# Kernel tuning notes

Measured on AMD Instinct MI355X. Metric: run time of the kernel, lower is better.

The kernel has to match this reference:

```python
import jax, jax.numpy as jnp
import numpy as np

B, C, H, W = 8, 512, 32, 32
NH = 8


def setup_inputs() -> dict:
    key = jax.random.key(0)
    ks = jax.random.split(key, 10)
    s = 1.0 / np.sqrt(C)
    return {
        "query": jax.random.normal(ks[0], (B, C, H, W), jnp.float32),
        "key": jax.random.normal(ks[1], (B, C, H, W), jnp.float32),
        "Wq": jax.random.normal(ks[2], (C, C), jnp.float32) * s,
        "bq": jnp.zeros((C,), jnp.float32),
        "Wk": jax.random.normal(ks[3], (C, C), jnp.float32) * s,
        "bk": jnp.zeros((C,), jnp.float32),
        "Wv": jax.random.normal(ks[4], (C, C), jnp.float32) * s,
        "bv": jnp.zeros((C,), jnp.float32),
        "Wo": jax.random.normal(ks[5], (C, C), jnp.float32) * s,
        "bo": jnp.zeros((C,), jnp.float32),
        "num_heads": NH,
    }


def reference(query, key, Wq, bq, Wk, bk, Wv, bv, Wo, bo, num_heads):
    b, c, h, w = query.shape
    hd = c // num_heads
    scale = hd ** (-0.5)
    # [B,C,H,W] -> [B, L, C] with L = H*W
    qf = jnp.transpose(query, (0, 2, 3, 1)).reshape(b, -1, c)
    kf = jnp.transpose(key, (0, 2, 3, 1)).reshape(b, -1, c)
    L = qf.shape[1]
    # Linear projections (torch Linear: x @ W.T + b); value = key
    q = qf @ Wq.T + bq
    k = kf @ Wk.T + bk
    v = kf @ Wv.T + bv
    # split heads: [B, L, NH, hd] -> [B, NH, L, hd]
    q = q.reshape(b, L, num_heads, hd).transpose(0, 2, 1, 3) * scale
    k = k.reshape(b, L, num_heads, hd).transpose(0, 2, 1, 3)
    v = v.reshape(b, L, num_heads, hd).transpose(0, 2, 1, 3)
    scores = jnp.einsum('bhqd,bhkd->bhqk', q, k)
    attn = jax.nn.softmax(scores, axis=-1)  # dropout p=0.0 -> identity
    o = jnp.einsum('bhqk,bhkd->bhqd', attn, v)
    o = o.transpose(0, 2, 1, 3).reshape(b, L, c)
    o = o @ Wo.T + bo
    o = o + qf + kf  # residual with flattened query and key
    return jnp.transpose(o.reshape(b, h, w, c), (0, 3, 1, 2))
```

## Files before the change

kernel.cpp:

```cpp
#include <hip/hip_runtime.h>
#include <stdint.h>

#define B_  8
#define C_  512
#define L_  1024
#define NH_ 8
#define HD_ 64

typedef __attribute__((ext_vector_type(8))) short short8;
typedef __attribute__((ext_vector_type(4))) short short4v;
typedef __attribute__((ext_vector_type(4))) float f32x4;
typedef __attribute__((ext_vector_type(2))) unsigned uint2v;

#define MFMA(a,b,c) __builtin_amdgcn_mfma_f32_16x16x32_bf16((a),(b),(c),0,0,0)
#define GLD16(g,l) __builtin_amdgcn_global_load_lds( \
    (const __attribute__((address_space(1))) void*)(g), \
    (__attribute__((address_space(3))) void*)(l), 16, 0, 0)

__device__ __forceinline__ unsigned short f2bf(float f) {
  union { float f; unsigned u; } x; x.f = f;
  unsigned r = x.u + 0x7FFFu + ((x.u >> 16) & 1u);
  return (unsigned short)(r >> 16);
}

__device__ __forceinline__ unsigned cvtpk_bf16(float lo, float hi) {
  unsigned r;
  asm("v_cvt_pk_bf16_f32 %0, %1, %2" : "=v"(r) : "v"(lo), "v"(hi));
  return r;
}

__global__ __launch_bounds__(256) void k_transpose(
    const float* __restrict__ q, const float* __restrict__ k,
    unsigned short* __restrict__ qf, unsigned short* __restrict__ kf) {
  __shared__ float t[32][33];
  const int z = blockIdx.z;
  const int b = z >> 1;
  const float* src = (z & 1) ? k : q;
  unsigned short* dst = (z & 1) ? kf : qf;
  const int tx = threadIdx.x & 31;
  const int ty = threadIdx.x >> 5;
  const int l0 = blockIdx.x * 32;
  const int c0 = blockIdx.y * 32;
#pragma unroll
  for (int i = 0; i < 4; ++i)
    t[ty + 8*i][tx] = src[((size_t)b * C_ + c0 + ty + 8*i) * L_ + l0 + tx];
  __syncthreads();
#pragma unroll
  for (int i = 0; i < 4; ++i)
    dst[((size_t)b * L_ + l0 + ty + 8*i) * C_ + c0 + tx] = f2bf(t[tx][ty + 8*i]);
}

__global__ __launch_bounds__(256) void k_convw(
    const float* __restrict__ w0, const float* __restrict__ w1,
    const float* __restrict__ w2, const float* __restrict__ w3,
    unsigned short* __restrict__ dst) {
  const int z = blockIdx.y;
  const float* s = (z == 0) ? w0 : (z == 1) ? w1 : (z == 2) ? w2 : w3;
  unsigned short* d = dst + (size_t)z * (C_ * C_);
  const int i = (blockIdx.x * 256 + threadIdx.x) * 4;
  float4 v = *(const float4*)&s[i];
  short4v p;
  p[0] = (short)f2bf(v.x); p[1] = (short)f2bf(v.y);
  p[2] = (short)f2bf(v.z); p[3] = (short)f2bf(v.w);
  *(short4v*)&d[i] = p;
}

template<int MREP>
__device__ __forceinline__ void gemm_core(
    const unsigned short* __restrict__ A, const unsigned short* __restrict__ W,
    const float* __restrict__ bias, void* __restrict__ outp,
    const float* __restrict__ resQ, const float* __restrict__ resK,
    int mode, float scale, unsigned short* lA, unsigned short* lB,
    int tm, int tn) {
  const int lane = threadIdx.x & 63;
  const int wid  = threadIdx.x >> 6;
  const int wm = wid >> 1, wn = wid & 1;
  const int r16 = lane & 15;
  const int g4  = lane >> 4;

  f32x4 acc[MREP][4];
#pragma unroll
  for (int i = 0; i < MREP; ++i)
#pragma unroll
    for (int j = 0; j < 4; ++j) acc[i][j] = (f32x4){0.f, 0.f, 0.f, 0.f};

  for (int kt = 0; kt < C_; kt += 64) {
#pragma unroll
    for (int i = 0; i < MREP; ++i) {
      int chunk = wid * MREP + i;
      int row = chunk * 8 + (lane >> 3);
      int col = (lane & 7) * 8;
      GLD16(A + (size_t)(tm + row) * C_ + kt + col, &lA[chunk * 512]);
    }
#pragma unroll
    for (int i = 0; i < 4; ++i) {
      int chunk = wid * 4 + i;
      int row = chunk * 8 + (lane >> 3);
      int col = (lane & 7) * 8;
      GLD16(W + (size_t)(tn + row) * C_ + kt + col, &lB[chunk * 512]);
    }
    __syncthreads();
#pragma unroll
    for (int ks = 0; ks < 2; ++ks) {
      const int co = ks * 32 + g4 * 8;
      short8 af[MREP], bw[4];
#pragma unroll
      for (int i = 0; i < MREP; ++i)
        af[i] = *(const short8*)&lA[(wm*(MREP*16) + i*16 + r16) * 64 + co];
#pragma unroll
      for (int j = 0; j < 4; ++j) bw[j] = *(const short8*)&lB[(wn*64 + j*16 + r16) * 64 + co];
#pragma unroll
      for (int i = 0; i < MREP; ++i)
#pragma unroll
        for (int j = 0; j < 4; ++j) acc[i][j] = MFMA(af[i], bw[j], acc[i][j]);
    }
    __syncthreads();
  }

  if (mode <= 1) {
    unsigned short* out = (unsigned short*)outp;
#pragma unroll
    for (int i = 0; i < MREP; ++i)
#pragma unroll
      for (int j = 0; j < 4; ++j) {
        int c = tn + wn*64 + j*16 + r16;
        float bia = bias[c];
        int h = c >> 6, d = c & 63;
#pragma unroll
        for (int r = 0; r < 4; ++r) {
          int gm = tm + wm*(MREP*16) + i*16 + g4*4 + r;
          int b = gm >> 10, l = gm & 1023;
          out[(((size_t)b * NH_ + h) * L_ + l) * HD_ + d] = f2bf((acc[i][j][r] + bia) * scale);
        }
      }
  } else if (mode == 2) {
    unsigned short* out = (unsigned short*)outp;
#pragma unroll
    for (int i = 0; i < MREP; ++i)
#pragma unroll
      for (int j = 0; j < 4; ++j) {
        int c = tn + wn*64 + j*16 + r16;
        float bia = bias[c];
        int h = c >> 6, d = c & 63;
        int gm0 = tm + wm*(MREP*16) + i*16 + g4*4;
        int b = gm0 >> 10, l0 = gm0 & 1023;
        short4v pk;
#pragma unroll
        for (int r = 0; r < 4; ++r) pk[r] = (short)f2bf(acc[i][j][r] + bia);
        *(short4v*)&out[(((size_t)b * NH_ + h) * HD_ + d) * L_ + l0] = pk;
      }
  } else {
    float* out = (float*)outp;
#pragma unroll
    for (int i = 0; i < MREP; ++i)
#pragma unroll
      for (int j = 0; j < 4; ++j) {
        int c = tn + wn*64 + j*16 + r16;
        float bia = bias[c];
        int gm0 = tm + wm*(MREP*16) + i*16 + g4*4;
        int b = gm0 >> 10, l0 = gm0 & 1023;
        size_t idx = ((size_t)b * C_ + c) * L_ + l0;
        float4 q4 = *(const float4*)&resQ[idx];
        float4 k4 = *(const float4*)&resK[idx];
        float4 o4;
        o4.x = acc[i][j][0] + bia + q4.x + k4.x;
        o4.y = acc[i][j][1] + bia + q4.y + k4.y;
        o4.z = acc[i][j][2] + bia + q4.z + k4.z;
        o4.w = acc[i][j][3] + bia + q4.w + k4.w;
        *(float4*)&out[idx] = o4;
      }
  }
}

__global__ __launch_bounds__(256) void k_proj(
    const unsigned short* __restrict__ qf, const unsigned short* __restrict__ kf,
    const unsigned short* __restrict__ Wqb, const unsigned short* __restrict__ Wkb,
    const unsigned short* __restrict__ Wvb,
    const float* __restrict__ bq, const float* __restrict__ bk, const float* __restrict__ bv,
    unsigned short* __restrict__ Qw, unsigned short* __restrict__ Kw,
    unsigned short* __restrict__ VTw) {
  __shared__ unsigned short lA[128 * 64];
  __shared__ unsigned short lB[128 * 64];
  const int bid = blockIdx.x;
  const int xcd = bid & 7;
  const int i_  = bid >> 3;
  const int ml  = i_ / 12;
  const int rem = i_ - ml * 12;
  const int z   = rem >> 2;
  const int n   = rem & 3;
  const int m   = xcd * 8 + ml;
  const unsigned short* A = (z == 0) ? qf : kf;
  const unsigned short* W = (z == 0) ? Wqb : (z == 1) ? Wkb : Wvb;
  const float* bias = (z == 0) ? bq : (z == 1) ? bk : bv;
  void* out = (z == 0) ? (void*)Qw : (z == 1) ? (void*)Kw : (void*)VTw;
  float scale = (z == 0) ? 0.125f * 1.44269504088896f : 1.0f;
  gemm_core<4>(A, W, bias, out, nullptr, nullptr, z, scale, lA, lB, m * 128, n * 128);
}

__global__ __launch_bounds__(256) void k_outproj(
    const unsigned short* __restrict__ O, const unsigned short* __restrict__ Wob,
    const float* __restrict__ bo, float* __restrict__ out,
    const float* __restrict__ query, const float* __restrict__ key) {
  __shared__ unsigned short lA[64 * 64];
  __shared__ unsigned short lB[128 * 64];
  const int bid = blockIdx.x;
  const int xcd = bid & 7;
  const int i_  = bid >> 3;
  const int m   = xcd * 16 + (i_ >> 2);
  const int n   = i_ & 3;
  gemm_core<2>(O, Wob, bo, out, query, key, 3, 1.0f, lA, lB, m * 64, n * 128);
}

__global__ __launch_bounds__(256, 2) void k_attn(
    const unsigned short* __restrict__ Q, const unsigned short* __restrict__ K,
    const unsigned short* __restrict__ VT, unsigned short* __restrict__ O) {
  __shared__ unsigned short Kt[2][64 * 64];
  __shared__ unsigned short Vt[2][64 * 64];
  __shared__ __align__(16) unsigned short Pl[4][32 * 36];
  const int lane = threadIdx.x & 63;
  const int wid  = threadIdx.x >> 6;
  const int bid  = blockIdx.x;
  const int xcd  = bid & 7;
  const int i_   = bid >> 3;
  const int bh   = xcd * 8 + (i_ >> 3);
  const int qb   = i_ & 7;
  const int qrow0 = qb * 128 + wid * 32;
  const int r16 = lane & 15;
  const int g4  = lane >> 4;
  const size_t base = (size_t)bh * L_ * HD_;
  const unsigned short* Kg = K + base;
  const unsigned short* Vg = VT + base;

  const int s0 = wid * 128 + lane;
  const int row0 = s0 >> 3,        ch0 = (s0 & 7) ^ (row0 & 7);
  const int row1 = (s0 + 64) >> 3, ch1 = ((s0 + 64) & 7) ^ (row1 & 7);

#define STAGE_KV(nxt, kt0) { \
    GLD16(Kg + (size_t)((kt0) + row0) * HD_ + ch0 * 8, &Kt[nxt][(wid*128)*8]); \
    GLD16(Kg + (size_t)((kt0) + row1) * HD_ + ch1 * 8, &Kt[nxt][(wid*128+64)*8]); \
    GLD16(Vg + (size_t)row0 * L_ + (kt0) + ch0 * 8, &Vt[nxt][(wid*128)*8]); \
    GLD16(Vg + (size_t)row1 * L_ + (kt0) + ch1 * 8, &Vt[nxt][(wid*128+64)*8]); \
  }

  short8 qv[2][2];
#pragma unroll
  for (int i = 0; i < 2; ++i)
#pragma unroll
    for (int ks = 0; ks < 2; ++ks)
      qv[i][ks] = *(const short8*)(Q + base + (size_t)(qrow0 + i*16 + r16) * HD_ + ks*32 + g4*8);

  short8 vones;
#pragma unroll
  for (int e = 0; e < 8; ++e) vones[e] = (short)0x3F80;

  f32x4 lacc[2];
  f32x4 oacc[2][4];
#pragma unroll
  for (int i = 0; i < 2; ++i) {
    lacc[i] = (f32x4){0.f, 0.f, 0.f, 0.f};
#pragma unroll
    for (int j = 0; j < 4; ++j) oacc[i][j] = (f32x4){0.f, 0.f, 0.f, 0.f};
  }

  unsigned short* myP = &Pl[wid][0];

  STAGE_KV(0, 0);
  __syncthreads();

  int cur = 0;
  for (int t = 0; t < 16; ++t) {
    if (t < 15) STAGE_KV(cur ^ 1, (t + 1) * 64);

    const unsigned short* lK = &Kt[cur][0];
    const unsigned short* lV = &Vt[cur][0];

    f32x4 sc[2][4];
#pragma unroll
    for (int i = 0; i < 2; ++i)
#pragma unroll
      for (int cf = 0; cf < 4; ++cf) sc[i][cf] = (f32x4){0.f, 0.f, 0.f, 0.f};

    const int swz = r16 & 7;
    __builtin_amdgcn_s_setprio(1);
#pragma unroll
    for (int cf = 0; cf < 4; ++cf) {
      const int rowb = (cf*16 + r16) * 64;
      short8 kb0 = *(const short8*)&lK[rowb + ((g4) ^ swz) * 8];
      short8 kb1 = *(const short8*)&lK[rowb + ((4 + g4) ^ swz) * 8];
      sc[0][cf] = MFMA(kb0, qv[0][0], sc[0][cf]);
      sc[0][cf] = MFMA(kb1, qv[0][1], sc[0][cf]);
      sc[1][cf] = MFMA(kb0, qv[1][0], sc[1][cf]);
      sc[1][cf] = MFMA(kb1, qv[1][1], sc[1][cf]);
    }
    __builtin_amdgcn_s_setprio(0);

#pragma unroll
    for (int half = 0; half < 2; ++half) {
#pragma unroll
      for (int i = 0; i < 2; ++i)
#pragma unroll
        for (int cfl = 0; cfl < 2; ++cfl) {
          const int cf = half * 2 + cfl;
          float p0 = exp2f(sc[i][cf][0]);
          float p1 = exp2f(sc[i][cf][1]);
          float p2 = exp2f(sc[i][cf][2]);
          float p3 = exp2f(sc[i][cf][3]);
          uint2v pk;
          pk[0] = cvtpk_bf16(p0, p1);
          pk[1] = cvtpk_bf16(p2, p3);
          *(uint2v*)&myP[(i*16 + r16) * 36 + cfl * 16 + g4 * 4] = pk;
        }
      short8 pa0 = *(const short8*)&myP[r16 * 36 + g4 * 8];
      short8 pa1 = *(const short8*)&myP[(16 + r16) * 36 + g4 * 8];
      __builtin_amdgcn_s_setprio(1);
      lacc[0] = MFMA(pa0, vones, lacc[0]);
      lacc[1] = MFMA(pa1, vones, lacc[1]);
#pragma unroll
      for (int j = 0; j < 4; ++j) {
        short8 vb = *(const short8*)&lV[(j*16 + r16) * 64 + ((half*4 + g4) ^ swz) * 8];
        oacc[0][j] = MFMA(pa0, vb, oacc[0][j]);
        oacc[1][j] = MFMA(pa1, vb, oacc[1][j]);
      }
      __builtin_amdgcn_s_setprio(0);
    }

    __syncthreads();
    cur ^= 1;
  }

  const int b = bh >> 3, h = bh & 7;
#pragma unroll
  for (int i = 0; i < 2; ++i) {
    float linv[4];
#pragma unroll
    for (int r = 0; r < 4; ++r) linv[r] = 1.0f / lacc[i][r];
#pragma unroll
    for (int j = 0; j < 4; ++j)
#pragma unroll
      for (int r = 0; r < 4; ++r) {
        int row = qrow0 + i*16 + g4*4 + r;
        int col = h*64 + j*16 + r16;
        O[((size_t)b * L_ + row) * C_ + col] = f2bf(oacc[i][j][r] * linv[r]);
      }
  }
#undef STAGE_KV
}

extern "C" void kernel_launch(void* const* d_in, const int* in_sizes, int n_in,
                              void* d_out, int out_size, void* d_ws, size_t ws_size,
                              hipStream_t stream) {
  (void)in_sizes; (void)n_in; (void)out_size; (void)ws_size;
  const float* query = (const float*)d_in[0];
  const float* key   = (const float*)d_in[1];
  const float* Wq = (const float*)d_in[2];
  const float* bq = (const float*)d_in[3];
  const float* Wk = (const float*)d_in[4];
  const float* bk = (const float*)d_in[5];
  const float* Wv = (const float*)d_in[6];
  const float* bv = (const float*)d_in[7];
  const float* Wo = (const float*)d_in[8];
  const float* bo = (const float*)d_in[9];

  char* ws = (char*)d_ws;
  unsigned short* qf  = (unsigned short*)(ws);
  unsigned short* kf  = (unsigned short*)(ws + 8388608);
  unsigned short* Wqb = (unsigned short*)(ws + 16777216);
  unsigned short* Wkb = Wqb + 262144;
  unsigned short* Wvb = Wkb + 262144;
  unsigned short* Wob = Wvb + 262144;
  unsigned short* Qw  = (unsigned short*)(ws + 18874368);
  unsigned short* Kw  = (unsigned short*)(ws + 27262976);
  unsigned short* VTw = (unsigned short*)(ws + 35651584);
  unsigned short* Ow  = (unsigned short*)(ws + 44040192);

  k_transpose<<<dim3(32, 16, 16), 256, 0, stream>>>(query, key, qf, kf);
  k_convw<<<dim3(256, 4), 256, 0, stream>>>(Wq, Wk, Wv, Wo, Wqb);
  k_proj<<<dim3(768), 256, 0, stream>>>(qf, kf, Wqb, Wkb, Wvb, bq, bk, bv, Qw, Kw, VTw);
  k_attn<<<dim3(512), 256, 0, stream>>>(Qw, Kw, VTw, Ow);
  k_outproj<<<dim3(512), 256, 0, stream>>>(Ow, Wob, bo, (float*)d_out, query, key);
}
```

Baseline: 102.2 us.

## Keep attention probabilities in registers via permuted K rows; merge weight conversion into transpose

The attention kernel drops the per-wave LDS round trip for the P matrix. It reorders which K rows each score MFMA reads, so the score accumulator layout already matches the A-operand layout of the PV MFMA, and it packs the exp2 results straight into bf16 registers. The weight bf16 conversion kernel is folded into the transpose kernel as an extra z-slice of blocks, which removes one launch. The risks are LDS bank conflicts from the new K row permutation and divergent block roles inside the transpose kernel.

```diff
diff --git a/kernel.cpp b/kernel.cpp
--- a/kernel.cpp
+++ b/kernel.cpp
@@ -31,9 +31,26 @@
 
 __global__ __launch_bounds__(256) void k_transpose(
     const float* __restrict__ q, const float* __restrict__ k,
-    unsigned short* __restrict__ qf, unsigned short* __restrict__ kf) {
+    unsigned short* __restrict__ qf, unsigned short* __restrict__ kf,
+    const float* __restrict__ w0, const float* __restrict__ w1,
+    const float* __restrict__ w2, const float* __restrict__ w3,
+    unsigned short* __restrict__ wdst) {
+  const int z = blockIdx.z;
+  if (z == 16) {
+    const int gb = blockIdx.y * 32 + blockIdx.x;
+    const float* s = (gb < 128) ? w0 : (gb < 256) ? w1 : (gb < 384) ? w2 : w3;
+    const int off = (gb & 127) * 2048 + threadIdx.x * 8;
+    float4 v0 = *(const float4*)&s[off];
+    float4 v1 = *(const float4*)&s[off + 4];
+    short8 p;
+    p[0] = (short)f2bf(v0.x); p[1] = (short)f2bf(v0.y);
+    p[2] = (short)f2bf(v0.z); p[3] = (short)f2bf(v0.w);
+    p[4] = (short)f2bf(v1.x); p[5] = (short)f2bf(v1.y);
+    p[6] = (short)f2bf(v1.z); p[7] = (short)f2bf(v1.w);
+    *(short8*)&wdst[(size_t)(gb >> 7) * 262144 + off] = p;
+    return;
+  }
   __shared__ float t[32][33];
-  const int z = blockIdx.z;
   const int b = z >> 1;
   const float* src = (z & 1) ? k : q;
   unsigned short* dst = (z & 1) ? kf : qf;
@@ -48,21 +65,6 @@
 #pragma unroll
   for (int i = 0; i < 4; ++i)
     dst[((size_t)b * L_ + l0 + ty + 8*i) * C_ + c0 + tx] = f2bf(t[tx][ty + 8*i]);
-}
-
-__global__ __launch_bounds__(256) void k_convw(
-    const float* __restrict__ w0, const float* __restrict__ w1,
-    const float* __restrict__ w2, const float* __restrict__ w3,
-    unsigned short* __restrict__ dst) {
-  const int z = blockIdx.y;
-  const float* s = (z == 0) ? w0 : (z == 1) ? w1 : (z == 2) ? w2 : w3;
-  unsigned short* d = dst + (size_t)z * (C_ * C_);
-  const int i = (blockIdx.x * 256 + threadIdx.x) * 4;
-  float4 v = *(const float4*)&s[i];
-  short4v p;
-  p[0] = (short)f2bf(v.x); p[1] = (short)f2bf(v.y);
-  p[2] = (short)f2bf(v.z); p[3] = (short)f2bf(v.w);
-  *(short4v*)&d[i] = p;
 }
 
 template<int MREP>
@@ -216,7 +218,6 @@
     const unsigned short* __restrict__ VT, unsigned short* __restrict__ O) {
   __shared__ unsigned short Kt[2][64 * 64];
   __shared__ unsigned short Vt[2][64 * 64];
-  __shared__ __align__(16) unsigned short Pl[4][32 * 36];
   const int lane = threadIdx.x & 63;
   const int wid  = threadIdx.x >> 6;
   const int bid  = blockIdx.x;
@@ -262,8 +263,6 @@
     for (int j = 0; j < 4; ++j) oacc[i][j] = (f32x4){0.f, 0.f, 0.f, 0.f};
   }
 
-  unsigned short* myP = &Pl[wid][0];
-
   STAGE_KV(0, 0);
   __syncthreads();
 
@@ -280,13 +279,15 @@
 #pragma unroll
       for (int cf = 0; cf < 4; ++cf) sc[i][cf] = (f32x4){0.f, 0.f, 0.f, 0.f};
 
-    const int swz = r16 & 7;
     __builtin_amdgcn_s_setprio(1);
 #pragma unroll
     for (int cf = 0; cf < 4; ++cf) {
-      const int rowb = (cf*16 + r16) * 64;
-      short8 kb0 = *(const short8*)&lK[rowb + ((g4) ^ swz) * 8];
-      short8 kb1 = *(const short8*)&lK[rowb + ((4 + g4) ^ swz) * 8];
+      const int h = cf >> 1, c = cf & 1;
+      const int rr = h*32 + ((r16 >> 2) << 3) + ((r16 & 3) << 1) + c;
+      const int s  = ((r16 & 3) << 1) + c;
+      const int rowb = rr * 64;
+      short8 kb0 = *(const short8*)&lK[rowb + ((g4) ^ s) * 8];
+      short8 kb1 = *(const short8*)&lK[rowb + ((4 + g4) ^ s) * 8];
       sc[0][cf] = MFMA(kb0, qv[0][0], sc[0][cf]);
       sc[0][cf] = MFMA(kb1, qv[0][1], sc[0][cf]);
       sc[1][cf] = MFMA(kb0, qv[1][0], sc[1][cf]);
@@ -294,30 +295,23 @@
     }
     __builtin_amdgcn_s_setprio(0);
 
-#pragma unroll
-    for (int half = 0; half < 2; ++half) {
-#pragma unroll
-      for (int i = 0; i < 2; ++i)
-#pragma unroll
-        for (int cfl = 0; cfl < 2; ++cfl) {
-          const int cf = half * 2 + cfl;
-          float p0 = exp2f(sc[i][cf][0]);
-          float p1 = exp2f(sc[i][cf][1]);
-          float p2 = exp2f(sc[i][cf][2]);
-          float p3 = exp2f(sc[i][cf][3]);
-          uint2v pk;
-          pk[0] = cvtpk_bf16(p0, p1);
-          pk[1] = cvtpk_bf16(p2, p3);
-          *(uint2v*)&myP[(i*16 + r16) * 36 + cfl * 16 + g4 * 4] = pk;
-        }
-      short8 pa0 = *(const short8*)&myP[r16 * 36 + g4 * 8];
-      short8 pa1 = *(const short8*)&myP[(16 + r16) * 36 + g4 * 8];
+    const int swz = r16 & 7;
+#pragma unroll
+    for (int h = 0; h < 2; ++h) {
+      union { unsigned u[4]; short8 s8; } pu0, pu1;
+#pragma unroll
+      for (int r = 0; r < 4; ++r) {
+        pu0.u[r] = cvtpk_bf16(exp2f(sc[0][h*2][r]), exp2f(sc[0][h*2+1][r]));
+        pu1.u[r] = cvtpk_bf16(exp2f(sc[1][h*2][r]), exp2f(sc[1][h*2+1][r]));
+      }
+      short8 pa0 = pu0.s8;
+      short8 pa1 = pu1.s8;
       __builtin_amdgcn_s_setprio(1);
       lacc[0] = MFMA(pa0, vones, lacc[0]);
       lacc[1] = MFMA(pa1, vones, lacc[1]);
 #pragma unroll
       for (int j = 0; j < 4; ++j) {
-        short8 vb = *(const short8*)&lV[(j*16 + r16) * 64 + ((half*4 + g4) ^ swz) * 8];
+        short8 vb = *(const short8*)&lV[(j*16 + r16) * 64 + ((h*4 + g4) ^ swz) * 8];
         oacc[0][j] = MFMA(pa0, vb, oacc[0][j]);
         oacc[1][j] = MFMA(pa1, vb, oacc[1][j]);
       }
@@ -373,8 +367,8 @@
   unsigned short* VTw = (unsigned short*)(ws + 35651584);
   unsigned short* Ow  = (unsigned short*)(ws + 44040192);
 
-  k_transpose<<<dim3(32, 16, 16), 256, 0, stream>>>(query, key, qf, kf);
-  k_convw<<<dim3(256, 4), 256, 0, stream>>>(Wq, Wk, Wv, Wo, Wqb);
+  k_transpose<<<dim3(32, 16, 17), 256, 0, stream>>>(query, key, qf, kf,
+                                                    Wq, Wk, Wv, Wo, Wqb);
   k_proj<<<dim3(768), 256, 0, stream>>>(qf, kf, Wqb, Wkb, Wvb, bq, bk, bv, Qw, Kw, VTw);
   k_attn<<<dim3(512), 256, 0, stream>>>(Qw, Kw, VTw, Ow);
   k_outproj<<<dim3(512), 256, 0, stream>>>(Ow, Wob, bo, (float*)d_out, query, key);
```

After: 93.04 us. 9.0% less time.
